# Performance work log

Measured on AMD Instinct MI355X. Metric: run time of the kernel, lower is better.

The kernel has to match this reference:

```python
import jax, jax.numpy as jnp
import numpy as np
from jax import lax

C = 512   # n_feat == Cn == Cdim (forced by DA_conv/CA_layer consistency)
H, W = 16, 32  # reshape_codebooks(512)
K = 3     # kernel_size
RED = 8   # reduction


def _lrelu(x):
    return jax.nn.leaky_relu(x, 0.1)


def _conv1x1(x, w, b=None):
    # x: (B,C,H,W), w: (O,C) -- torch Conv2d(.,.,1) weight squeezed
    y = jnp.einsum('oc,bchw->bohw', w, x)
    if b is not None:
        y = y + b[None, :, None, None]
    return y


def _conv3x3(x, w, b):
    # x: (B,C,H,W), w: (O,C,3,3) OIHW, padding=k//2 == SAME for odd k
    y = lax.conv_general_dilated(x, w, (1, 1), 'SAME',
                                 dimension_numbers=('NCHW', 'OIHW', 'NCHW'))
    return y + b[None, :, None, None]


def _da_conv(c, deg, kw1, kw2, pw, pb, caw1, caw2):
    # per-channel dynamic kernels from degradation vectors: (Cn, K*K)
    kern = (_lrelu(deg @ kw1.T) @ kw2.T).reshape(C, 1, K, K)
    # depthwise conv, groups = b1*c1 = C (b1 == 1)
    out = lax.conv_general_dilated(c, kern, (1, 1), 'SAME',
                                   feature_group_count=C,
                                   dimension_numbers=('NCHW', 'OIHW', 'NCHW'))
    out = _lrelu(out)
    out = _conv1x1(out, pw, pb)
    # CA_layer: deg reshaped to (1, Cn, 16, 32), channel attention, deg * att
    dr = deg.reshape(1, C, H, W)
    att = jax.nn.sigmoid(_conv1x1(_lrelu(_conv1x1(dr, caw1)), caw2))
    return out + dr * att


def setup_inputs() -> dict:
    key = jax.random.key(0)
    ks = jax.random.split(key, 16)
    n = lambda i, shape, s=0.05: jax.random.normal(ks[i], shape, dtype=jnp.float32) * s
    return dict(
        c=jax.random.normal(ks[0], (1, C, H, W), dtype=jnp.float32),
        deg=jax.random.normal(ks[1], (C, C), dtype=jnp.float32) * 0.1,
        k1_w1=n(2, (C, C)), k1_w2=n(3, (K * K, C)),
        p1_w=n(4, (C, C)), p1_b=jnp.zeros((C,), jnp.float32),
        ca1_w1=n(5, (C // RED, C)), ca1_w2=n(6, (C, C // RED)),
        conv1_w=n(7, (C, C, K, K)), conv1_b=jnp.zeros((C,), jnp.float32),
        k2_w1=n(8, (C, C)), k2_w2=n(9, (K * K, C)),
        p2_w=n(10, (C, C)), p2_b=jnp.zeros((C,), jnp.float32),
        ca2_w1=n(11, (C // RED, C)), ca2_w2=n(12, (C, C // RED)),
        conv2_w=n(13, (C, C, K, K)), conv2_b=jnp.zeros((C,), jnp.float32),
    )


def reference(c, deg, k1_w1, k1_w2, p1_w, p1_b, ca1_w1, ca1_w2,
              conv1_w, conv1_b, k2_w1, k2_w2, p2_w, p2_b,
              ca2_w1, ca2_w2, conv2_w, conv2_b):
    out = _lrelu(_da_conv(c, deg, k1_w1, k1_w2, p1_w, p1_b, ca1_w1, ca1_w2))
    out = _lrelu(_conv3x3(out, conv1_w, conv1_b))
    out = _lrelu(_da_conv(out, deg, k2_w1, k2_w2, p2_w, p2_b, ca2_w1, ca2_w2))
    return _conv3x3(out, conv2_w, conv2_b) + c
```

## Files before the change

kernel.cpp:

```cpp
#include <hip/hip_runtime.h>
#include <hip/hip_bf16.h>

typedef __attribute__((ext_vector_type(8))) unsigned short ushort8;
typedef __attribute__((ext_vector_type(8))) __bf16 bf16x8;
typedef __attribute__((ext_vector_type(4))) float f32x4;
typedef __attribute__((ext_vector_type(4))) unsigned short ushort4v;

__device__ __forceinline__ float lrelu_f(float v){ return v > 0.f ? v : 0.1f*v; }

__device__ __forceinline__ unsigned short f2bf(float v){
  unsigned u = __float_as_uint(v);
  unsigned r = (u + 0x7fffu + ((u>>16)&1u)) >> 16;
  return (unsigned short)r;
}
__device__ __forceinline__ float bf2f(unsigned short u){
  return __uint_as_float(((unsigned)u)<<16);
}

__device__ __forceinline__ void packq(const float* __restrict__ s,
                                      unsigned short* __restrict__ d, int i){
  const float4 v = ((const float4*)s)[i];
  ushort4v o; o.x=f2bf(v.x); o.y=f2bf(v.y); o.z=f2bf(v.z); o.w=f2bf(v.w);
  *(ushort4v*)(d + (size_t)i*4) = o;
}

__global__ __launch_bounds__(256) void k_pack_all(
  const float* __restrict__ k1_w1, const float* __restrict__ k2_w1,
  const float* __restrict__ p1_w,  const float* __restrict__ p2_w,
  const float* __restrict__ ca1_w1,const float* __restrict__ ca1_w2,
  const float* __restrict__ ca2_w1,const float* __restrict__ ca2_w2,
  const float* __restrict__ deg,   const float* __restrict__ conv1_w,
  const float* __restrict__ conv2_w,
  unsigned short* __restrict__ K1B, unsigned short* __restrict__ K2B,
  unsigned short* __restrict__ P1B, unsigned short* __restrict__ P2B,
  unsigned short* __restrict__ CA1A,unsigned short* __restrict__ CA1B,
  unsigned short* __restrict__ CA2A,unsigned short* __restrict__ CA2B,
  unsigned short* __restrict__ DEGB,unsigned short* __restrict__ DEGT,
  unsigned short* __restrict__ WB1, unsigned short* __restrict__ WB2){
  int i = blockIdx.x*256 + threadIdx.x;
  if (i < 65536){ packq(k1_w1, K1B, i); return; } i -= 65536;
  if (i < 65536){ packq(k2_w1, K2B, i); return; } i -= 65536;
  if (i < 65536){ packq(p1_w,  P1B, i); return; } i -= 65536;
  if (i < 65536){ packq(p2_w,  P2B, i); return; } i -= 65536;
  if (i < 8192){ packq(ca1_w1, CA1A, i); return; } i -= 8192;
  if (i < 8192){ packq(ca1_w2, CA1B, i); return; } i -= 8192;
  if (i < 8192){ packq(ca2_w1, CA2A, i); return; } i -= 8192;
  if (i < 8192){ packq(ca2_w2, CA2B, i); return; } i -= 8192;
  if (i < 65536){ packq(deg, DEGB, i); return; } i -= 65536;
  if (i < 65536){
    const int j = i*4; const int p = j>>9, c = j&511;
    ushort4v o;
    o.x = f2bf(deg[(size_t)(c+0)*512 + p]);
    o.y = f2bf(deg[(size_t)(c+1)*512 + p]);
    o.z = f2bf(deg[(size_t)(c+2)*512 + p]);
    o.w = f2bf(deg[(size_t)(c+3)*512 + p]);
    *(ushort4v*)(DEGT + (size_t)j) = o;
    return;
  } i -= 65536;
  if (i < 589824){
    const int o_ = i/1152; const int r4 = (i - o_*1152)*4;
    const int t = r4>>9; const int ci = r4&511;
    const float* s = conv1_w + (size_t)o_*4608;
    ushort4v o;
    o.x = f2bf(s[(ci+0)*9 + t]); o.y = f2bf(s[(ci+1)*9 + t]);
    o.z = f2bf(s[(ci+2)*9 + t]); o.w = f2bf(s[(ci+3)*9 + t]);
    *(ushort4v*)(WB1 + (size_t)o_*4608 + r4) = o;
    return;
  } i -= 589824;
  if (i < 589824){
    const int o_ = i/1152; const int r4 = (i - o_*1152)*4;
    const int t = r4>>9; const int ci = r4&511;
    const float* s = conv2_w + (size_t)o_*4608;
    ushort4v o;
    o.x = f2bf(s[(ci+0)*9 + t]); o.y = f2bf(s[(ci+1)*9 + t]);
    o.z = f2bf(s[(ci+2)*9 + t]); o.w = f2bf(s[(ci+3)*9 + t]);
    *(ushort4v*)(WB2 + (size_t)o_*4608 + r4) = o;
  }
}

__device__ __forceinline__ void gemm64(
    const unsigned short* __restrict__ A, const unsigned short* __restrict__ Bt,
    int m0, int n0, int K, int tid,
    unsigned short* lA, unsigned short* lB, f32x4 acc[2][2]){
  const int wid = tid>>6, lane = tid&63;
  const int srow = tid>>2, skb = tid&3;
  const unsigned short* gA = A  + (size_t)(m0+srow)*K + skb*8;
  const unsigned short* gB = Bt + (size_t)(n0+srow)*K + skb*8;
  const int soff = srow*32 + 8*(skb ^ (srow&3));
  const int wr = (wid>>1)*32, wc = (wid&1)*32;
  const int l15 = lane&15, lkb = lane>>4;
  int aoff[2], boff[2];
  #pragma unroll
  for (int s=0;s<2;s++){
    const int Ra = wr + s*16 + l15;
    aoff[s] = Ra*32 + 8*(lkb ^ (Ra&3));
    const int Rb = wc + s*16 + l15;
    boff[s] = Rb*32 + 8*(lkb ^ (Rb&3));
  }
  const int nst = K>>5;
  ushort8 ra = *(const ushort8*)gA;
  ushort8 rb = *(const ushort8*)gB;
  *(ushort8*)(lA + soff) = ra;
  *(ushort8*)(lB + soff) = rb;
  if (nst > 1){ ra = *(const ushort8*)(gA+32); rb = *(const ushort8*)(gB+32); }
  __syncthreads();
  for (int st=0; st<nst; ++st){
    const int cur = (st&1)*2048;
    bf16x8 af[2], bfr[2];
    #pragma unroll
    for (int s=0;s<2;s++){
      af[s]  = *(const bf16x8*)(lA + cur + aoff[s]);
      bfr[s] = *(const bf16x8*)(lB + cur + boff[s]);
    }
    if (st+1 < nst){
      const int nxt = ((st+1)&1)*2048;
      *(ushort8*)(lA + nxt + soff) = ra;
      *(ushort8*)(lB + nxt + soff) = rb;
      if (st+2 < nst){
        ra = *(const ushort8*)(gA + (size_t)(st+2)*32);
        rb = *(const ushort8*)(gB + (size_t)(st+2)*32);
      }
    }
    #pragma unroll
    for (int mi=0;mi<2;mi++)
      #pragma unroll
      for (int ni=0;ni<2;ni++)
        acc[mi][ni] = __builtin_amdgcn_mfma_f32_16x16x32_bf16(af[mi], bfr[ni], acc[mi][ni], 0,0,0);
    __syncthreads();
  }
}

__global__ __launch_bounds__(256) void k_prep(
    const unsigned short* __restrict__ DEGB, const unsigned short* __restrict__ DEGT,
    const unsigned short* __restrict__ K1B,  const unsigned short* __restrict__ K2B,
    const unsigned short* __restrict__ CA1A, const unsigned short* __restrict__ CA2A,
    const unsigned short* __restrict__ CA1B, const unsigned short* __restrict__ CA2B,
    const float* __restrict__ kw2a, const float* __restrict__ kw2b,
    float* __restrict__ KP1, float* __restrict__ KP2,
    float* __restrict__ ATT1, float* __restrict__ ATT2){
  __shared__ unsigned short lA[4096], lB[4096];
  __shared__ float kp[2][64][9];
  __shared__ unsigned short hid[4096];
  int bid = blockIdx.x;
  const int tid = threadIdx.x;
  const int wid = tid>>6, lane = tid&63;
  const int l15 = lane&15, lkb = lane>>4;

  if (bid < 128){
    const int b  = bid>>6;
    const int r6 = bid&63;
    const int it = r6>>3, jc = r6&7;
    const unsigned short* Bt = b ? K2B : K1B;
    const float* kw2 = b ? kw2b : kw2a;
    float* KP = b ? KP2 : KP1;
    f32x4 acc[2][2] = {};
    gemm64(DEGB, Bt, it*64, jc*64, 512, tid, lA, lB, acc);

    const int wr = (wid>>1)*32, wcl = wid&1;
    const int col0 = wcl*32 + l15, col1 = col0 + 16;
    float w0[9], w1[9];
    #pragma unroll
    for (int t=0;t<9;t++){
      w0[t] = kw2[t*512 + jc*64 + col0];
      w1[t] = kw2[t*512 + jc*64 + col1];
    }
    #pragma unroll
    for (int mi=0;mi<2;mi++)
      #pragma unroll
      for (int r=0;r<4;r++){
        const float v0 = lrelu_f(acc[mi][0][r]);
        const float v1 = lrelu_f(acc[mi][1][r]);
        const int row = wr + mi*16 + lkb*4 + r;
        #pragma unroll
        for (int t=0;t<9;t++){
          float p = v0*w0[t] + v1*w1[t];
          p += __shfl_xor(p,1); p += __shfl_xor(p,2);
          p += __shfl_xor(p,4); p += __shfl_xor(p,8);
          if (l15==0) kp[wcl][row][t] = p;
        }
      }
    __syncthreads();
    for (int i = tid; i < 576; i += 256){
      const int row = i/9, t = i - row*9;
      KP[((size_t)jc*512 + it*64 + row)*9 + t] = kp[0][row][t] + kp[1][row][t];
    }
  } else {
    bid -= 128;
    const int b  = bid>>6;
    const int r6 = bid&63;
    const int mt = r6>>3, pt = r6&7;
    const unsigned short* CAa = b ? CA2A : CA1A;
    const unsigned short* CAb = b ? CA2B : CA1B;
    float* ATT = b ? ATT2 : ATT1;
    f32x4 acc[2][2] = {};
    gemm64(DEGT, CAa, pt*64, 0, 512, tid, lA, lB, acc);

    const int wr = (wid>>1)*32, wc = (wid&1)*32;
    #pragma unroll
    for (int mi=0;mi<2;mi++)
      #pragma unroll
      for (int ni=0;ni<2;ni++)
        #pragma unroll
        for (int r=0;r<4;r++){
          const int row = wr + mi*16 + lkb*4 + r;
          const int col = wc + ni*16 + l15;
          hid[row*64 + 8*((col>>3) ^ (row&7)) + (col&7)] = f2bf(lrelu_f(acc[mi][ni][r]));
        }
    __syncthreads();
    const int arow = tid>>2, akb0 = (tid&3)*2;
    #pragma unroll
    for (int kk=0;kk<2;kk++){
      const int kb = akb0+kk;
      *(ushort8*)(lA + arow*64 + 8*(kb ^ (arow&7))) =
        *(const ushort8*)(CAb + (size_t)(mt*64+arow)*64 + kb*8);
    }
    __syncthreads();
    f32x4 a2[2][2] = {};
    #pragma unroll
    for (int h=0;h<2;h++){
      bf16x8 af2[2], bf2[2];
      #pragma unroll
      for (int mi=0;mi<2;mi++){
        const int Ra = wr + mi*16 + l15;
        af2[mi] = *(const bf16x8*)(lA + Ra*64 + 8*((h*4+lkb) ^ (Ra&7)));
      }
      #pragma unroll
      for (int ni=0;ni<2;ni++){
        const int Rb = wc + ni*16 + l15;
        bf2[ni] = *(const bf16x8*)(hid + Rb*64 + 8*((h*4+lkb) ^ (Rb&7)));
      }
      #pragma unroll
      for (int mi=0;mi<2;mi++)
        #pragma unroll
        for (int ni=0;ni<2;ni++)
          a2[mi][ni] = __builtin_amdgcn_mfma_f32_16x16x32_bf16(af2[mi], bf2[ni], a2[mi][ni], 0,0,0);
    }
    #pragma unroll
    for (int mi=0;mi<2;mi++)
      #pragma unroll
      for (int ni=0;ni<2;ni++)
        #pragma unroll
        for (int r=0;r<4;r++){
          const int row = mt*64 + wr + mi*16 + lkb*4 + r;
          const int col = pt*64 + wc + ni*16 + l15;
          ATT[(size_t)row*512 + col] = 1.f/(1.f + expf(-a2[mi][ni][r]));
        }
  }
}

__global__ __launch_bounds__(512) void k_dwconv(const float* __restrict__ x,
    const float* __restrict__ KP, unsigned short* __restrict__ yt){
  const int c = blockIdx.x;
  const int p = threadIdx.x;
  const int iy = p>>5, ix = p&31;
  __shared__ float plane[18*34];
  __shared__ float ks[9];
  for (int i=p;i<18*34;i+=512) plane[i]=0.f;
  if (p < 9){
    float s = 0.f;
    #pragma unroll
    for (int jc=0;jc<8;jc++) s += KP[((size_t)jc*512 + c)*9 + p];
    ks[p] = s;
  }
  __syncthreads();
  plane[(iy+1)*34 + ix+1] = x[c*512 + p];
  __syncthreads();
  float s = 0.f;
  #pragma unroll
  for (int dy=0;dy<3;dy++)
    #pragma unroll
    for (int dx=0;dx<3;dx++)
      s += plane[(iy+dy)*34 + ix+dx]*ks[dy*3+dx];
  yt[(size_t)p*512 + c] = f2bf(lrelu_f(s));
}

__global__ __launch_bounds__(512) void k_dwconv_red(const unsigned short* __restrict__ part,
    const float* __restrict__ bias, const float* __restrict__ KP,
    unsigned short* __restrict__ yt, int nchunks){
  const int c = blockIdx.x;
  const int p = threadIdx.x;
  const int iy = p>>5, ix = p&31;
  __shared__ float plane[18*34];
  __shared__ float ks[9];
  for (int i=p;i<18*34;i+=512) plane[i]=0.f;
  if (p < 9){
    float s = 0.f;
    #pragma unroll
    for (int jc=0;jc<8;jc++) s += KP[((size_t)jc*512 + c)*9 + p];
    ks[p] = s;
  }
  __syncthreads();
  if (p < 128){
    const float b = bias[c];
    float4 a4 = {b,b,b,b};
    for (int s=0;s<nchunks;s++){
      const ushort4v v = ((const ushort4v*)(part + (size_t)s*262144 + c*512))[p];
      a4.x += bf2f(v.x); a4.y += bf2f(v.y); a4.z += bf2f(v.z); a4.w += bf2f(v.w);
    }
    a4.x = lrelu_f(a4.x); a4.y = lrelu_f(a4.y);
    a4.z = lrelu_f(a4.z); a4.w = lrelu_f(a4.w);
    const int px0 = p*4;
    float* dst = &plane[((px0>>5)+1)*34 + (px0&31)+1];
    dst[0]=a4.x; dst[1]=a4.y; dst[2]=a4.z; dst[3]=a4.w;
  }
  __syncthreads();
  float s = 0.f;
  #pragma unroll
  for (int dy=0;dy<3;dy++)
    #pragma unroll
    for (int dx=0;dx<3;dx++)
      s += plane[(iy+dy)*34 + ix+dx]*ks[dy*3+dx];
  yt[(size_t)p*512 + c] = f2bf(lrelu_f(s));
}

__global__ __launch_bounds__(256) void k_pw(
    const unsigned short* __restrict__ A, const unsigned short* __restrict__ Bt,
    const float* __restrict__ bias,
    const float* __restrict__ E1, const float* __restrict__ E2,
    unsigned short* __restrict__ XT){
  __shared__ unsigned short lA[2][1024], lB[2][1024];
  __shared__ float tile[32][33];
  const int tid = threadIdx.x;
  const int wid = tid>>6, lane = tid&63;
  const int M0 = blockIdx.x*32, N0 = blockIdx.y*32;

  const int half = tid>>7;
  const int st_ = tid&127;
  const int srow = st_>>2, skb = st_&3;
  const unsigned short* gS = (half ? Bt + (size_t)(N0+srow)*512
                                   : A  + (size_t)(M0+srow)*512) + skb*8;
  unsigned short (*lS)[1024] = half ? lB : lA;
  const int soff = srow*32 + 8*(skb ^ (srow&3));

  const int wr = (wid>>1)*16, wc = (wid&1)*16;
  const int l15 = lane&15, lkb = lane>>4;
  const int Ra = wr + l15, Rb = wc + l15;
  const int aoff = Ra*32 + 8*(lkb ^ (Ra&3));
  const int boff = Rb*32 + 8*(lkb ^ (Rb&3));

  f32x4 acc = {};
  ushort8 r0 = *(const ushort8*)gS;
  *(ushort8*)(&lS[0][soff]) = r0;
  r0 = *(const ushort8*)(gS+32);
  __syncthreads();
  for (int st=0; st<16; ++st){
    const int cur = st&1;
    const bf16x8 af = *(const bf16x8*)(&lA[cur][aoff]);
    const bf16x8 bf = *(const bf16x8*)(&lB[cur][boff]);
    if (st+1 < 16){
      *(ushort8*)(&lS[cur^1][soff]) = r0;
      if (st+2 < 16) r0 = *(const ushort8*)(gS + (size_t)(st+2)*32);
    }
    acc = __builtin_amdgcn_mfma_f32_16x16x32_bf16(af, bf, acc, 0,0,0);
    __syncthreads();
  }

  #pragma unroll
  for (int r=0;r<4;r++){
    const int rl = wr + lkb*4 + r;
    const int cl = wc + l15;
    const int rr = M0 + rl, col = N0 + cl;
    float v = acc[r] + bias[rr] + E1[(size_t)rr*512+col]*E2[(size_t)rr*512+col];
    tile[rl][cl] = lrelu_f(v);
  }
  __syncthreads();
  const int pr = tid>>3, q = tid&7;
  ushort4v o;
  o.x = f2bf(tile[q*4+0][pr]); o.y = f2bf(tile[q*4+1][pr]);
  o.z = f2bf(tile[q*4+2][pr]); o.w = f2bf(tile[q*4+3][pr]);
  *(ushort4v*)(XT + (size_t)(N0+pr)*512 + M0 + q*4) = o;
}

template<int KCH>
__global__ __launch_bounds__(256) void k_mfma_conv(
    const unsigned short* __restrict__ WB,
    const unsigned short* __restrict__ XT,
    unsigned short* __restrict__ part){
  __shared__ unsigned short lA[2][4096];
  __shared__ unsigned short lB[2][8192];
  const int tid = threadIdx.x;
  const int wid = tid>>6, lane = tid&63;
  const int m0 = blockIdx.x*64, n0 = blockIdx.y*128;
  const int k0 = blockIdx.z*KCH;

  const int srow = tid>>2, skb = tid&3;
  const unsigned short* gA = WB + (size_t)(m0+srow)*4608 + k0 + skb*8;
  const int brow1 = srow + 64;
  const int p0 = n0 + srow, p1 = n0 + brow1;
  const int py0 = p0>>5, px0 = p0&31, py1 = p1>>5, px1 = p1&31;
  const int s7 = srow&7;
  const int soffA0 = srow*64 + 8*(skb ^ s7);
  const int soffA1 = srow*64 + 8*((skb+4) ^ s7);
  const int soffB00 = soffA0,            soffB01 = soffA1;
  const int soffB10 = brow1*64 + 8*(skb ^ s7);
  const int soffB11 = brow1*64 + 8*((skb+4) ^ s7);

  const int wr = (wid>>1)*32, wc = (wid&1)*64;
  const int l15 = lane&15, lkb = lane>>4;
  int aoff[2][2], boff[4][2];
  #pragma unroll
  for (int s=0;s<2;s++){
    const int Ra = wr + s*16 + l15;
    #pragma unroll
    for (int h=0;h<2;h++) aoff[s][h] = Ra*64 + 8*((lkb+4*h) ^ (Ra&7));
  }
  #pragma unroll
  for (int u=0;u<4;u++){
    const int Rb = wc + u*16 + l15;
    #pragma unroll
    for (int h=0;h<2;h++) boff[u][h] = Rb*64 + 8*((lkb+4*h) ^ (Rb&7));
  }

  auto ldB = [&](int st, int py, int px, ushort8& lo, ushort8& hi){
    const int k = k0 + st*64;
    const int t = k>>9;
    const int dy = t/3, dx = t - dy*3;
    const int yy = py + dy - 1, xx = px + dx - 1;
    lo = (ushort8){}; hi = (ushort8){};
    if ((unsigned)yy < 16u && (unsigned)xx < 32u){
      const unsigned short* b = XT + (size_t)(yy*32+xx)*512 + (k&511) + skb*8;
      lo = *(const ushort8*)b; hi = *(const ushort8*)(b+32);
    }
  };

  constexpr int NST = KCH/64;
  f32x4 acc[2][4] = {};
  ushort8 ra0 = *(const ushort8*)gA;
  ushort8 ra1 = *(const ushort8*)(gA+32);
  ushort8 b00,b01,b10,b11;
  ldB(0, py0, px0, b00, b01);
  ldB(0, py1, px1, b10, b11);
  *(ushort8*)(&lA[0][soffA0]) = ra0;  *(ushort8*)(&lA[0][soffA1]) = ra1;
  *(ushort8*)(&lB[0][soffB00]) = b00; *(ushort8*)(&lB[0][soffB01]) = b01;
  *(ushort8*)(&lB[0][soffB10]) = b10; *(ushort8*)(&lB[0][soffB11]) = b11;
  if (NST > 1){
    ra0 = *(const ushort8*)(gA+64); ra1 = *(const ushort8*)(gA+96);
    ldB(1, py0, px0, b00, b01);
    ldB(1, py1, px1, b10, b11);
  }
  __syncthreads();
  for (int st=0; st<NST; ++st){
    const int cur = st&1;
    bf16x8 af[2][2], bfr[4][2];
    #pragma unroll
    for (int s=0;s<2;s++)
      #pragma unroll
      for (int h=0;h<2;h++) af[s][h] = *(const bf16x8*)(&lA[cur][aoff[s][h]]);
    #pragma unroll
    for (int u=0;u<4;u++)
      #pragma unroll
      for (int h=0;h<2;h++) bfr[u][h] = *(const bf16x8*)(&lB[cur][boff[u][h]]);
    if (st+1 < NST){
      const int nxt = cur^1;
      *(ushort8*)(&lA[nxt][soffA0]) = ra0;  *(ushort8*)(&lA[nxt][soffA1]) = ra1;
      *(ushort8*)(&lB[nxt][soffB00]) = b00; *(ushort8*)(&lB[nxt][soffB01]) = b01;
      *(ushort8*)(&lB[nxt][soffB10]) = b10; *(ushort8*)(&lB[nxt][soffB11]) = b11;
      if (st+2 < NST){
        ra0 = *(const ushort8*)(gA + (size_t)(st+2)*64);
        ra1 = *(const ushort8*)(gA + (size_t)(st+2)*64 + 32);
        ldB(st+2, py0, px0, b00, b01);
        ldB(st+2, py1, px1, b10, b11);
      }
    }
    #pragma unroll
    for (int h=0;h<2;h++)
      #pragma unroll
      for (int s=0;s<2;s++)
        #pragma unroll
        for (int u=0;u<4;u++)
          acc[s][u] = __builtin_amdgcn_mfma_f32_16x16x32_bf16(af[s][h], bfr[u][h], acc[s][u], 0,0,0);
    __syncthreads();
  }

  unsigned short* pbase = part + (size_t)blockIdx.z*262144;
  #pragma unroll
  for (int s=0;s<2;s++)
    #pragma unroll
    for (int u=0;u<4;u++){
      const int row = m0 + wr + s*16 + lkb*4;
      const int col = n0 + wc + u*16 + l15;
      #pragma unroll
      for (int r=0;r<4;r++)
        pbase[(size_t)(row+r)*512 + col] = f2bf(acc[s][u][r]);
    }
}

__global__ __launch_bounds__(256) void k_reduce_final(const unsigned short* __restrict__ part,
    const float* __restrict__ bias, const float* __restrict__ res,
    float* __restrict__ y, int nchunks){
  const int i = blockIdx.x*256 + threadIdx.x;
  const int o = i>>7;
  const float b = bias[o];
  float4 a4 = {b,b,b,b};
  for (int s=0;s<nchunks;s++){
    const ushort4v v = ((const ushort4v*)part)[(size_t)s*65536 + i];
    a4.x += bf2f(v.x); a4.y += bf2f(v.y); a4.z += bf2f(v.z); a4.w += bf2f(v.w);
  }
  const float4 rv = ((const float4*)res)[i];
  a4.x += rv.x; a4.y += rv.y; a4.z += rv.z; a4.w += rv.w;
  ((float4*)y)[i] = a4;
}

extern "C" void kernel_launch(void* const* d_in, const int* in_sizes, int n_in,
                              void* d_out, int out_size, void* d_ws, size_t ws_size,
                              hipStream_t stream) {
  (void)in_sizes; (void)n_in; (void)out_size; (void)ws_size;
  const float* xin    = (const float*)d_in[0];
  const float* deg    = (const float*)d_in[1];
  const float* k1_w1  = (const float*)d_in[2];
  const float* k1_w2  = (const float*)d_in[3];
  const float* p1_w   = (const float*)d_in[4];
  const float* p1_b   = (const float*)d_in[5];
  const float* ca1_w1 = (const float*)d_in[6];
  const float* ca1_w2 = (const float*)d_in[7];
  const float* conv1_w= (const float*)d_in[8];
  const float* conv1_b= (const float*)d_in[9];
  const float* k2_w1  = (const float*)d_in[10];
  const float* k2_w2  = (const float*)d_in[11];
  const float* p2_w   = (const float*)d_in[12];
  const float* p2_b   = (const float*)d_in[13];
  const float* ca2_w1 = (const float*)d_in[14];
  const float* ca2_w2 = (const float*)d_in[15];
  const float* conv2_w= (const float*)d_in[16];
  const float* conv2_b= (const float*)d_in[17];
  float* out = (float*)d_out;

  const int NS = 18;

  float* ws = (float*)d_ws;
  unsigned short* PART = (unsigned short*)ws;
  ws += (size_t)NS*131072;
  float* KP1  = ws;  ws += 36864;
  float* KP2  = ws;  ws += 36864;
  float* ATT1 = ws;  ws += 262144;
  float* ATT2 = ws;  ws += 262144;
  unsigned short* DEGB = (unsigned short*)ws; ws += 131072;
  unsigned short* DEGT = (unsigned short*)ws; ws += 131072;
  unsigned short* K1B  = (unsigned short*)ws; ws += 131072;
  unsigned short* K2B  = (unsigned short*)ws; ws += 131072;
  unsigned short* P1B  = (unsigned short*)ws; ws += 131072;
  unsigned short* P2B  = (unsigned short*)ws; ws += 131072;
  unsigned short* CA1A = (unsigned short*)ws; ws += 16384;
  unsigned short* CA1B = (unsigned short*)ws; ws += 16384;
  unsigned short* CA2A = (unsigned short*)ws; ws += 16384;
  unsigned short* CA2B = (unsigned short*)ws; ws += 16384;
  unsigned short* DWLT = (unsigned short*)ws; ws += 131072;
  unsigned short* XT   = (unsigned short*)ws; ws += 131072;
  unsigned short* WB1  = (unsigned short*)ws; ws += 1179648;
  unsigned short* WB2  = (unsigned short*)ws; ws += 1179648;

  k_pack_all<<<6272,256,0,stream>>>(k1_w1,k2_w1,p1_w,p2_w,
      ca1_w1,ca1_w2,ca2_w1,ca2_w2, deg, conv1_w, conv2_w,
      K1B,K2B,P1B,P2B, CA1A,CA1B,CA2A,CA2B, DEGB,DEGT, WB1,WB2);

  k_prep<<<256,256,0,stream>>>(DEGB,DEGT, K1B,K2B, CA1A,CA2A, CA1B,CA2B,
      k1_w2,k2_w2, KP1,KP2, ATT1,ATT2);

  k_dwconv<<<512,512,0,stream>>>(xin, KP1, DWLT);
  k_pw<<<dim3(16,16),256,0,stream>>>(P1B, DWLT, p1_b, deg, ATT1, XT);
  k_mfma_conv<256><<<dim3(8,4,18),256,0,stream>>>(WB1, XT, PART);
  k_dwconv_red<<<512,512,0,stream>>>(PART, conv1_b, KP2, DWLT, NS);
  k_pw<<<dim3(16,16),256,0,stream>>>(P2B, DWLT, p2_b, deg, ATT2, XT);
  k_mfma_conv<256><<<dim3(8,4,18),256,0,stream>>>(WB2, XT, PART);
  k_reduce_final<<<256,256,0,stream>>>(PART, conv2_b, xin, out, NS);
}
```

Baseline: 87.80 us.

## Fuse all stages into one cooperative persistent kernel with grid syncs

```diff
diff --git a/kernel.cpp b/kernel.cpp
--- a/kernel.cpp
+++ b/kernel.cpp
@@ -1,5 +1,8 @@
 #include <hip/hip_runtime.h>
 #include <hip/hip_bf16.h>
+#include <hip/hip_cooperative_groups.h>
+
+namespace cg = cooperative_groups;
 
 typedef __attribute__((ext_vector_type(8))) unsigned short ushort8;
 typedef __attribute__((ext_vector_type(8))) __bf16 bf16x8;
@@ -24,59 +27,18 @@
   *(ushort4v*)(d + (size_t)i*4) = o;
 }
 
-__global__ __launch_bounds__(256) void k_pack_all(
-  const float* __restrict__ k1_w1, const float* __restrict__ k2_w1,
-  const float* __restrict__ p1_w,  const float* __restrict__ p2_w,
-  const float* __restrict__ ca1_w1,const float* __restrict__ ca1_w2,
-  const float* __restrict__ ca2_w1,const float* __restrict__ ca2_w2,
-  const float* __restrict__ deg,   const float* __restrict__ conv1_w,
-  const float* __restrict__ conv2_w,
-  unsigned short* __restrict__ K1B, unsigned short* __restrict__ K2B,
-  unsigned short* __restrict__ P1B, unsigned short* __restrict__ P2B,
-  unsigned short* __restrict__ CA1A,unsigned short* __restrict__ CA1B,
-  unsigned short* __restrict__ CA2A,unsigned short* __restrict__ CA2B,
-  unsigned short* __restrict__ DEGB,unsigned short* __restrict__ DEGT,
-  unsigned short* __restrict__ WB1, unsigned short* __restrict__ WB2){
-  int i = blockIdx.x*256 + threadIdx.x;
-  if (i < 65536){ packq(k1_w1, K1B, i); return; } i -= 65536;
-  if (i < 65536){ packq(k2_w1, K2B, i); return; } i -= 65536;
-  if (i < 65536){ packq(p1_w,  P1B, i); return; } i -= 65536;
-  if (i < 65536){ packq(p2_w,  P2B, i); return; } i -= 65536;
-  if (i < 8192){ packq(ca1_w1, CA1A, i); return; } i -= 8192;
-  if (i < 8192){ packq(ca1_w2, CA1B, i); return; } i -= 8192;
-  if (i < 8192){ packq(ca2_w1, CA2A, i); return; } i -= 8192;
-  if (i < 8192){ packq(ca2_w2, CA2B, i); return; } i -= 8192;
-  if (i < 65536){ packq(deg, DEGB, i); return; } i -= 65536;
-  if (i < 65536){
-    const int j = i*4; const int p = j>>9, c = j&511;
-    ushort4v o;
-    o.x = f2bf(deg[(size_t)(c+0)*512 + p]);
-    o.y = f2bf(deg[(size_t)(c+1)*512 + p]);
-    o.z = f2bf(deg[(size_t)(c+2)*512 + p]);
-    o.w = f2bf(deg[(size_t)(c+3)*512 + p]);
-    *(ushort4v*)(DEGT + (size_t)j) = o;
-    return;
-  } i -= 65536;
-  if (i < 589824){
-    const int o_ = i/1152; const int r4 = (i - o_*1152)*4;
-    const int t = r4>>9; const int ci = r4&511;
-    const float* s = conv1_w + (size_t)o_*4608;
-    ushort4v o;
-    o.x = f2bf(s[(ci+0)*9 + t]); o.y = f2bf(s[(ci+1)*9 + t]);
-    o.z = f2bf(s[(ci+2)*9 + t]); o.w = f2bf(s[(ci+3)*9 + t]);
-    *(ushort4v*)(WB1 + (size_t)o_*4608 + r4) = o;
-    return;
-  } i -= 589824;
-  if (i < 589824){
-    const int o_ = i/1152; const int r4 = (i - o_*1152)*4;
-    const int t = r4>>9; const int ci = r4&511;
-    const float* s = conv2_w + (size_t)o_*4608;
-    ushort4v o;
-    o.x = f2bf(s[(ci+0)*9 + t]); o.y = f2bf(s[(ci+1)*9 + t]);
-    o.z = f2bf(s[(ci+2)*9 + t]); o.w = f2bf(s[(ci+3)*9 + t]);
-    *(ushort4v*)(WB2 + (size_t)o_*4608 + r4) = o;
-  }
-}
+struct Prm {
+  const float *xin,*deg;
+  const float *k1_w1,*k1_w2,*p1_b,*conv1_b;
+  const float *k2_w1,*k2_w2,*p2_b,*conv2_b;
+  const float *p1_w,*p2_w,*ca1_w1,*ca1_w2,*ca2_w1,*ca2_w2,*conv1_w,*conv2_w;
+  float* out;
+  unsigned short *PART,*DEGB,*DEGT,*K1B,*K2B,*P1B,*P2B;
+  unsigned short *CA1A,*CA1B,*CA2A,*CA2B,*DWLT,*XT,*WB1,*WB2;
+  float *KP1,*KP2,*ATT1,*ATT2;
+};
+
+#define NT_TOTAL 65536
 
 __device__ __forceinline__ void gemm64(
     const unsigned short* __restrict__ A, const unsigned short* __restrict__ Bt,
@@ -130,17 +92,47 @@
   }
 }
 
-__global__ __launch_bounds__(256) void k_prep(
-    const unsigned short* __restrict__ DEGB, const unsigned short* __restrict__ DEGT,
-    const unsigned short* __restrict__ K1B,  const unsigned short* __restrict__ K2B,
-    const unsigned short* __restrict__ CA1A, const unsigned short* __restrict__ CA2A,
-    const unsigned short* __restrict__ CA1B, const unsigned short* __restrict__ CA2B,
-    const float* __restrict__ kw2a, const float* __restrict__ kw2b,
-    float* __restrict__ KP1, float* __restrict__ KP2,
-    float* __restrict__ ATT1, float* __restrict__ ATT2){
-  __shared__ unsigned short lA[4096], lB[4096];
-  __shared__ float kp[2][64][9];
-  __shared__ unsigned short hid[4096];
+__device__ __forceinline__ void ph_pack(const Prm& p){
+  const int g0 = blockIdx.x*256 + threadIdx.x;
+  for (int i = g0; i < 1605632; i += NT_TOTAL){
+    int j = i;
+    if (j < 65536){ packq(p.k1_w1, p.K1B, j); continue; } j -= 65536;
+    if (j < 65536){ packq(p.k2_w1, p.K2B, j); continue; } j -= 65536;
+    if (j < 65536){ packq(p.p1_w,  p.P1B, j); continue; } j -= 65536;
+    if (j < 65536){ packq(p.p2_w,  p.P2B, j); continue; } j -= 65536;
+    if (j < 8192){ packq(p.ca1_w1, p.CA1A, j); continue; } j -= 8192;
+    if (j < 8192){ packq(p.ca1_w2, p.CA1B, j); continue; } j -= 8192;
+    if (j < 8192){ packq(p.ca2_w1, p.CA2A, j); continue; } j -= 8192;
+    if (j < 8192){ packq(p.ca2_w2, p.CA2B, j); continue; } j -= 8192;
+    if (j < 65536){ packq(p.deg, p.DEGB, j); continue; } j -= 65536;
+    if (j < 65536){
+      const int q = j*4; const int px = q>>9, c = q&511;
+      ushort4v o;
+      o.x = f2bf(p.deg[(size_t)(c+0)*512 + px]);
+      o.y = f2bf(p.deg[(size_t)(c+1)*512 + px]);
+      o.z = f2bf(p.deg[(size_t)(c+2)*512 + px]);
+      o.w = f2bf(p.deg[(size_t)(c+3)*512 + px]);
+      *(ushort4v*)(p.DEGT + (size_t)q) = o;
+      continue;
+    } j -= 65536;
+    const float* src; unsigned short* dst;
+    if (j < 589824){ src = p.conv1_w; dst = p.WB1; }
+    else { j -= 589824; src = p.conv2_w; dst = p.WB2; }
+    const int o_ = j/1152; const int r4 = (j - o_*1152)*4;
+    const int t = r4>>9; const int ci = r4&511;
+    const float* s = src + (size_t)o_*4608;
+    ushort4v o;
+    o.x = f2bf(s[(ci+0)*9 + t]); o.y = f2bf(s[(ci+1)*9 + t]);
+    o.z = f2bf(s[(ci+2)*9 + t]); o.w = f2bf(s[(ci+3)*9 + t]);
+    *(ushort4v*)(dst + (size_t)o_*4608 + r4) = o;
+  }
+}
+
+__device__ __forceinline__ void ph_prep(const Prm& p, unsigned char* smem){
+  unsigned short* lA = (unsigned short*)smem;
+  unsigned short* lB = lA + 4096;
+  float* kpf = (float*)(smem + 16384);
+  unsigned short* hid = (unsigned short*)(smem + 21056);
   int bid = blockIdx.x;
   const int tid = threadIdx.x;
   const int wid = tid>>6, lane = tid&63;
@@ -150,11 +142,11 @@
     const int b  = bid>>6;
     const int r6 = bid&63;
     const int it = r6>>3, jc = r6&7;
-    const unsigned short* Bt = b ? K2B : K1B;
-    const float* kw2 = b ? kw2b : kw2a;
-    float* KP = b ? KP2 : KP1;
+    const unsigned short* Bt = b ? p.K2B : p.K1B;
+    const float* kw2 = b ? p.k2_w2 : p.k1_w2;
+    float* KP = b ? p.KP2 : p.KP1;
     f32x4 acc[2][2] = {};
-    gemm64(DEGB, Bt, it*64, jc*64, 512, tid, lA, lB, acc);
+    gemm64(p.DEGB, Bt, it*64, jc*64, 512, tid, lA, lB, acc);
 
     const int wr = (wid>>1)*32, wcl = wid&1;
     const int col0 = wcl*32 + l15, col1 = col0 + 16;
@@ -173,27 +165,27 @@
         const int row = wr + mi*16 + lkb*4 + r;
         #pragma unroll
         for (int t=0;t<9;t++){
-          float p = v0*w0[t] + v1*w1[t];
-          p += __shfl_xor(p,1); p += __shfl_xor(p,2);
-          p += __shfl_xor(p,4); p += __shfl_xor(p,8);
-          if (l15==0) kp[wcl][row][t] = p;
+          float q = v0*w0[t] + v1*w1[t];
+          q += __shfl_xor(q,1); q += __shfl_xor(q,2);
+          q += __shfl_xor(q,4); q += __shfl_xor(q,8);
+          if (l15==0) kpf[wcl*576 + row*9 + t] = q;
         }
       }
     __syncthreads();
     for (int i = tid; i < 576; i += 256){
       const int row = i/9, t = i - row*9;
-      KP[((size_t)jc*512 + it*64 + row)*9 + t] = kp[0][row][t] + kp[1][row][t];
+      KP[((size_t)jc*512 + it*64 + row)*9 + t] = kpf[row*9+t] + kpf[576 + row*9+t];
     }
   } else {
     bid -= 128;
     const int b  = bid>>6;
     const int r6 = bid&63;
     const int mt = r6>>3, pt = r6&7;
-    const unsigned short* CAa = b ? CA2A : CA1A;
-    const unsigned short* CAb = b ? CA2B : CA1B;
-    float* ATT = b ? ATT2 : ATT1;
+    const unsigned short* CAa = b ? p.CA2A : p.CA1A;
+    const unsigned short* CAb = b ? p.CA2B : p.CA1B;
+    float* ATT = b ? p.ATT2 : p.ATT1;
     f32x4 acc[2][2] = {};
-    gemm64(DEGT, CAa, pt*64, 0, 512, tid, lA, lB, acc);
+    gemm64(p.DEGT, CAa, pt*64, 0, 512, tid, lA, lB, acc);
 
     const int wr = (wid>>1)*32, wc = (wid&1)*32;
     #pragma unroll
@@ -248,88 +240,76 @@
   }
 }
 
-__global__ __launch_bounds__(512) void k_dwconv(const float* __restrict__ x,
-    const float* __restrict__ KP, unsigned short* __restrict__ yt){
-  const int c = blockIdx.x;
-  const int p = threadIdx.x;
-  const int iy = p>>5, ix = p&31;
-  __shared__ float plane[18*34];
-  __shared__ float ks[9];
-  for (int i=p;i<18*34;i+=512) plane[i]=0.f;
-  if (p < 9){
-    float s = 0.f;
-    #pragma unroll
-    for (int jc=0;jc<8;jc++) s += KP[((size_t)jc*512 + c)*9 + p];
-    ks[p] = s;
-  }
-  __syncthreads();
-  plane[(iy+1)*34 + ix+1] = x[c*512 + p];
-  __syncthreads();
-  float s = 0.f;
+template<int MODE>
+__device__ __forceinline__ void ph_dw(const Prm& p, const float* KP,
+    const float* bias, unsigned char* smem){
+  float* plane = (float*)smem;
+  float* ks = plane + 612;
+  const int tid = threadIdx.x;
+  for (int i=tid;i<612;i+=256) plane[i]=0.f;
   #pragma unroll
-  for (int dy=0;dy<3;dy++)
-    #pragma unroll
-    for (int dx=0;dx<3;dx++)
-      s += plane[(iy+dy)*34 + ix+dx]*ks[dy*3+dx];
-  yt[(size_t)p*512 + c] = f2bf(lrelu_f(s));
-}
-
-__global__ __launch_bounds__(512) void k_dwconv_red(const unsigned short* __restrict__ part,
-    const float* __restrict__ bias, const float* __restrict__ KP,
-    unsigned short* __restrict__ yt, int nchunks){
-  const int c = blockIdx.x;
-  const int p = threadIdx.x;
-  const int iy = p>>5, ix = p&31;
-  __shared__ float plane[18*34];
-  __shared__ float ks[9];
-  for (int i=p;i<18*34;i+=512) plane[i]=0.f;
-  if (p < 9){
-    float s = 0.f;
-    #pragma unroll
-    for (int jc=0;jc<8;jc++) s += KP[((size_t)jc*512 + c)*9 + p];
-    ks[p] = s;
-  }
-  __syncthreads();
-  if (p < 128){
-    const float b = bias[c];
-    float4 a4 = {b,b,b,b};
-    for (int s=0;s<nchunks;s++){
-      const ushort4v v = ((const ushort4v*)(part + (size_t)s*262144 + c*512))[p];
-      a4.x += bf2f(v.x); a4.y += bf2f(v.y); a4.z += bf2f(v.z); a4.w += bf2f(v.w);
-    }
-    a4.x = lrelu_f(a4.x); a4.y = lrelu_f(a4.y);
-    a4.z = lrelu_f(a4.z); a4.w = lrelu_f(a4.w);
-    const int px0 = p*4;
-    float* dst = &plane[((px0>>5)+1)*34 + (px0&31)+1];
-    dst[0]=a4.x; dst[1]=a4.y; dst[2]=a4.z; dst[3]=a4.w;
-  }
-  __syncthreads();
-  float s = 0.f;
-  #pragma unroll
-  for (int dy=0;dy<3;dy++)
-    #pragma unroll
-    for (int dx=0;dx<3;dx++)
-      s += plane[(iy+dy)*34 + ix+dx]*ks[dy*3+dx];
-  yt[(size_t)p*512 + c] = f2bf(lrelu_f(s));
-}
-
-__global__ __launch_bounds__(256) void k_pw(
-    const unsigned short* __restrict__ A, const unsigned short* __restrict__ Bt,
-    const float* __restrict__ bias,
-    const float* __restrict__ E1, const float* __restrict__ E2,
-    unsigned short* __restrict__ XT){
-  __shared__ unsigned short lA[2][1024], lB[2][1024];
-  __shared__ float tile[32][33];
+  for (int cc=0; cc<2; ++cc){
+    const int c = blockIdx.x*2 + cc;
+    __syncthreads();
+    if (tid<9){
+      float s=0.f;
+      #pragma unroll
+      for (int jc=0;jc<8;jc++) s += KP[((size_t)jc*512 + c)*9 + tid];
+      ks[tid]=s;
+    }
+    if constexpr (MODE==0){
+      #pragma unroll
+      for (int q=0;q<2;q++){
+        const int px = tid + q*256;
+        plane[((px>>5)+1)*34 + (px&31)+1] = p.xin[(size_t)c*512 + px];
+      }
+    } else {
+      if (tid < 128){
+        const float b = bias[c];
+        float4 a4 = {b,b,b,b};
+        #pragma unroll
+        for (int s=0;s<4;s++){
+          const ushort4v v = ((const ushort4v*)(p.PART + (size_t)s*262144 + c*512))[tid];
+          a4.x += bf2f(v.x); a4.y += bf2f(v.y); a4.z += bf2f(v.z); a4.w += bf2f(v.w);
+        }
+        a4.x = lrelu_f(a4.x); a4.y = lrelu_f(a4.y);
+        a4.z = lrelu_f(a4.z); a4.w = lrelu_f(a4.w);
+        const int px0 = tid*4;
+        float* dst = &plane[((px0>>5)+1)*34 + (px0&31)+1];
+        dst[0]=a4.x; dst[1]=a4.y; dst[2]=a4.z; dst[3]=a4.w;
+      }
+    }
+    __syncthreads();
+    #pragma unroll
+    for (int q=0;q<2;q++){
+      const int px = tid + q*256;
+      const int iy = px>>5, ix = px&31;
+      float s = 0.f;
+      #pragma unroll
+      for (int dy=0;dy<3;dy++)
+        #pragma unroll
+        for (int dx=0;dx<3;dx++)
+          s += plane[(iy+dy)*34 + ix+dx]*ks[dy*3+dx];
+      p.DWLT[(size_t)px*512 + c] = f2bf(lrelu_f(s));
+    }
+  }
+}
+
+__device__ __forceinline__ void ph_pw(const Prm& p, const unsigned short* A,
+    const float* bias, const float* ATT, unsigned char* smem){
+  unsigned short* lA = (unsigned short*)smem;
+  unsigned short* lB = lA + 2048;
+  float* tile = (float*)(smem + 8192);
   const int tid = threadIdx.x;
   const int wid = tid>>6, lane = tid&63;
-  const int M0 = blockIdx.x*32, N0 = blockIdx.y*32;
+  const int M0 = (blockIdx.x&15)*32, N0 = (blockIdx.x>>4)*32;
 
   const int half = tid>>7;
   const int st_ = tid&127;
   const int srow = st_>>2, skb = st_&3;
-  const unsigned short* gS = (half ? Bt + (size_t)(N0+srow)*512
-                                   : A  + (size_t)(M0+srow)*512) + skb*8;
-  unsigned short (*lS)[1024] = half ? lB : lA;
+  const unsigned short* gS = (half ? p.DWLT + (size_t)(N0+srow)*512
+                                   : A      + (size_t)(M0+srow)*512) + skb*8;
+  unsigned short* lS = half ? lB : lA;
   const int soff = srow*32 + 8*(skb ^ (srow&3));
 
   const int wr = (wid>>1)*16, wc = (wid&1)*16;
@@ -340,15 +320,15 @@
 
   f32x4 acc = {};
   ushort8 r0 = *(const ushort8*)gS;
-  *(ushort8*)(&lS[0][soff]) = r0;
+  *(ushort8*)(lS + soff) = r0;
   r0 = *(const ushort8*)(gS+32);
   __syncthreads();
   for (int st=0; st<16; ++st){
-    const int cur = st&1;
-    const bf16x8 af = *(const bf16x8*)(&lA[cur][aoff]);
-    const bf16x8 bf = *(const bf16x8*)(&lB[cur][boff]);
+    const int cur = (st&1)*1024;
+    const bf16x8 af = *(const bf16x8*)(lA + cur + aoff);
+    const bf16x8 bf = *(const bf16x8*)(lB + cur + boff);
     if (st+1 < 16){
-      *(ushort8*)(&lS[cur^1][soff]) = r0;
+      *(ushort8*)(lS + (cur^1024) + soff) = r0;
       if (st+2 < 16) r0 = *(const ushort8*)(gS + (size_t)(st+2)*32);
     }
     acc = __builtin_amdgcn_mfma_f32_16x16x32_bf16(af, bf, acc, 0,0,0);
@@ -360,207 +340,221 @@
     const int rl = wr + lkb*4 + r;
     const int cl = wc + l15;
     const int rr = M0 + rl, col = N0 + cl;
-    float v = acc[r] + bias[rr] + E1[(size_t)rr*512+col]*E2[(size_t)rr*512+col];
-    tile[rl][cl] = lrelu_f(v);
+    float v = acc[r] + bias[rr] + p.deg[(size_t)rr*512+col]*ATT[(size_t)rr*512+col];
+    tile[rl*33 + cl] = lrelu_f(v);
   }
   __syncthreads();
   const int pr = tid>>3, q = tid&7;
   ushort4v o;
-  o.x = f2bf(tile[q*4+0][pr]); o.y = f2bf(tile[q*4+1][pr]);
-  o.z = f2bf(tile[q*4+2][pr]); o.w = f2bf(tile[q*4+3][pr]);
-  *(ushort4v*)(XT + (size_t)(N0+pr)*512 + M0 + q*4) = o;
-}
-
-template<int KCH>
-__global__ __launch_bounds__(256) void k_mfma_conv(
-    const unsigned short* __restrict__ WB,
-    const unsigned short* __restrict__ XT,
-    unsigned short* __restrict__ part){
-  __shared__ unsigned short lA[2][4096];
-  __shared__ unsigned short lB[2][8192];
+  o.x = f2bf(tile[(q*4+0)*33 + pr]); o.y = f2bf(tile[(q*4+1)*33 + pr]);
+  o.z = f2bf(tile[(q*4+2)*33 + pr]); o.w = f2bf(tile[(q*4+3)*33 + pr]);
+  *(ushort4v*)(p.XT + (size_t)(N0+pr)*512 + M0 + q*4) = o;
+}
+
+__device__ __forceinline__ void ph_conv(const Prm& p, const unsigned short* WB,
+    unsigned char* smem){
+  unsigned short* lA = (unsigned short*)smem;
+  unsigned short* lB = lA + 8192;
   const int tid = threadIdx.x;
+  const int bid = blockIdx.x;
+  const int z = bid & 3, ny = (bid>>2)&7, mx = bid>>5;
+  const int m0 = mx*64, n0 = ny*64, k0 = z*1152;
   const int wid = tid>>6, lane = tid&63;
-  const int m0 = blockIdx.x*64, n0 = blockIdx.y*128;
-  const int k0 = blockIdx.z*KCH;
-
   const int srow = tid>>2, skb = tid&3;
   const unsigned short* gA = WB + (size_t)(m0+srow)*4608 + k0 + skb*8;
-  const int brow1 = srow + 64;
-  const int p0 = n0 + srow, p1 = n0 + brow1;
-  const int py0 = p0>>5, px0 = p0&31, py1 = p1>>5, px1 = p1&31;
+  const int pp = n0 + srow, py = pp>>5, px = pp&31;
   const int s7 = srow&7;
-  const int soffA0 = srow*64 + 8*(skb ^ s7);
-  const int soffA1 = srow*64 + 8*((skb+4) ^ s7);
-  const int soffB00 = soffA0,            soffB01 = soffA1;
-  const int soffB10 = brow1*64 + 8*(skb ^ s7);
-  const int soffB11 = brow1*64 + 8*((skb+4) ^ s7);
-
-  const int wr = (wid>>1)*32, wc = (wid&1)*64;
+  const int soff0 = srow*64 + 8*(skb ^ s7);
+  const int soff1 = srow*64 + 8*((skb+4) ^ s7);
+
+  const int wr = (wid>>1)*32, wc = (wid&1)*32;
   const int l15 = lane&15, lkb = lane>>4;
-  int aoff[2][2], boff[4][2];
+  int aoff[2][2], boff[2][2];
   #pragma unroll
   for (int s=0;s<2;s++){
     const int Ra = wr + s*16 + l15;
-    #pragma unroll
-    for (int h=0;h<2;h++) aoff[s][h] = Ra*64 + 8*((lkb+4*h) ^ (Ra&7));
-  }
-  #pragma unroll
-  for (int u=0;u<4;u++){
-    const int Rb = wc + u*16 + l15;
-    #pragma unroll
-    for (int h=0;h<2;h++) boff[u][h] = Rb*64 + 8*((lkb+4*h) ^ (Rb&7));
-  }
-
-  auto ldB = [&](int st, int py, int px, ushort8& lo, ushort8& hi){
+    const int Rb = wc + s*16 + l15;
+    #pragma unroll
+    for (int h=0;h<2;h++){
+      aoff[s][h] = Ra*64 + 8*((lkb+4*h) ^ (Ra&7));
+      boff[s][h] = Rb*64 + 8*((lkb+4*h) ^ (Rb&7));
+    }
+  }
+
+  auto ldB = [&](int st, ushort8& lo, ushort8& hi){
     const int k = k0 + st*64;
     const int t = k>>9;
     const int dy = t/3, dx = t - dy*3;
     const int yy = py + dy - 1, xx = px + dx - 1;
     lo = (ushort8){}; hi = (ushort8){};
     if ((unsigned)yy < 16u && (unsigned)xx < 32u){
-      const unsigned short* b = XT + (size_t)(yy*32+xx)*512 + (k&511) + skb*8;
+      const unsigned short* b = p.XT + (size_t)(yy*32+xx)*512 + (k&511) + skb*8;
       lo = *(const ushort8*)b; hi = *(const ushort8*)(b+32);
     }
   };
 
-  constexpr int NST = KCH/64;
-  f32x4 acc[2][4] = {};
+  constexpr int NST = 18;
+  f32x4 acc[2][2] = {};
   ushort8 ra0 = *(const ushort8*)gA;
   ushort8 ra1 = *(const ushort8*)(gA+32);
-  ushort8 b00,b01,b10,b11;
-  ldB(0, py0, px0, b00, b01);
-  ldB(0, py1, px1, b10, b11);
-  *(ushort8*)(&lA[0][soffA0]) = ra0;  *(ushort8*)(&lA[0][soffA1]) = ra1;
-  *(ushort8*)(&lB[0][soffB00]) = b00; *(ushort8*)(&lB[0][soffB01]) = b01;
-  *(ushort8*)(&lB[0][soffB10]) = b10; *(ushort8*)(&lB[0][soffB11]) = b11;
-  if (NST > 1){
-    ra0 = *(const ushort8*)(gA+64); ra1 = *(const ushort8*)(gA+96);
-    ldB(1, py0, px0, b00, b01);
-    ldB(1, py1, px1, b10, b11);
-  }
+  ushort8 b0, b1;
+  ldB(0, b0, b1);
+  *(ushort8*)(lA + soff0) = ra0; *(ushort8*)(lA + soff1) = ra1;
+  *(ushort8*)(lB + soff0) = b0;  *(ushort8*)(lB + soff1) = b1;
+  ra0 = *(const ushort8*)(gA+64); ra1 = *(const ushort8*)(gA+96);
+  ldB(1, b0, b1);
   __syncthreads();
   for (int st=0; st<NST; ++st){
-    const int cur = st&1;
-    bf16x8 af[2][2], bfr[4][2];
+    const int cur = (st&1)*4096;
+    bf16x8 af[2][2], bfr[2][2];
     #pragma unroll
     for (int s=0;s<2;s++)
       #pragma unroll
-      for (int h=0;h<2;h++) af[s][h] = *(const bf16x8*)(&lA[cur][aoff[s][h]]);
-    #pragma unroll
-    for (int u=0;u<4;u++)
-      #pragma unroll
-      for (int h=0;h<2;h++) bfr[u][h] = *(const bf16x8*)(&lB[cur][boff[u][h]]);
+      for (int h=0;h<2;h++){
+        af[s][h]  = *(const bf16x8*)(lA + cur + aoff[s][h]);
+        bfr[s][h] = *(const bf16x8*)(lB + cur + boff[s][h]);
+      }
     if (st+1 < NST){
-      const int nxt = cur^1;
-      *(ushort8*)(&lA[nxt][soffA0]) = ra0;  *(ushort8*)(&lA[nxt][soffA1]) = ra1;
-      *(ushort8*)(&lB[nxt][soffB00]) = b00; *(ushort8*)(&lB[nxt][soffB01]) = b01;
-      *(ushort8*)(&lB[nxt][soffB10]) = b10; *(ushort8*)(&lB[nxt][soffB11]) = b11;
+      const int nxt = cur ^ 4096;
+      *(ushort8*)(lA + nxt + soff0) = ra0; *(ushort8*)(lA + nxt + soff1) = ra1;
+      *(ushort8*)(lB + nxt + soff0) = b0;  *(ushort8*)(lB + nxt + soff1) = b1;
       if (st+2 < NST){
         ra0 = *(const ushort8*)(gA + (size_t)(st+2)*64);
         ra1 = *(const ushort8*)(gA + (size_t)(st+2)*64 + 32);
-        ldB(st+2, py0, px0, b00, b01);
-        ldB(st+2, py1, px1, b10, b11);
+        ldB(st+2, b0, b1);
       }
     }
     #pragma unroll
     for (int h=0;h<2;h++)
       #pragma unroll
-      for (int s=0;s<2;s++)
-        #pragma unroll
-        for (int u=0;u<4;u++)
-          acc[s][u] = __builtin_amdgcn_mfma_f32_16x16x32_bf16(af[s][h], bfr[u][h], acc[s][u], 0,0,0);
-    __syncthreads();
-  }
-
-  unsigned short* pbase = part + (size_t)blockIdx.z*262144;
+      for (int mi=0;mi<2;mi++)
+        #pragma unroll
+        for (int ni=0;ni<2;ni++)
+          acc[mi][ni] = __builtin_amdgcn_mfma_f32_16x16x32_bf16(af[mi][h], bfr[ni][h], acc[mi][ni], 0,0,0);
+    __syncthreads();
+  }
+
+  unsigned short* pbase = p.PART + (size_t)z*262144;
   #pragma unroll
-  for (int s=0;s<2;s++)
-    #pragma unroll
-    for (int u=0;u<4;u++){
-      const int row = m0 + wr + s*16 + lkb*4;
-      const int col = n0 + wc + u*16 + l15;
+  for (int mi=0;mi<2;mi++)
+    #pragma unroll
+    for (int ni=0;ni<2;ni++){
+      const int row = m0 + wr + mi*16 + lkb*4;
+      const int col = n0 + wc + ni*16 + l15;
       #pragma unroll
       for (int r=0;r<4;r++)
-        pbase[(size_t)(row+r)*512 + col] = f2bf(acc[s][u][r]);
-    }
-}
-
-__global__ __launch_bounds__(256) void k_reduce_final(const unsigned short* __restrict__ part,
-    const float* __restrict__ bias, const float* __restrict__ res,
-    float* __restrict__ y, int nchunks){
-  const int i = blockIdx.x*256 + threadIdx.x;
-  const int o = i>>7;
-  const float b = bias[o];
+        pbase[(size_t)(row+r)*512 + col] = f2bf(acc[mi][ni][r]);
+    }
+}
+
+__device__ __forceinline__ void ph_reduce(const Prm& p){
+  const int gid = blockIdx.x*256 + threadIdx.x;
+  const int o = gid>>7;
+  const float b = p.conv2_b[o];
   float4 a4 = {b,b,b,b};
-  for (int s=0;s<nchunks;s++){
-    const ushort4v v = ((const ushort4v*)part)[(size_t)s*65536 + i];
+  #pragma unroll
+  for (int s=0;s<4;s++){
+    const ushort4v v = ((const ushort4v*)p.PART)[(size_t)s*65536 + gid];
     a4.x += bf2f(v.x); a4.y += bf2f(v.y); a4.z += bf2f(v.z); a4.w += bf2f(v.w);
   }
-  const float4 rv = ((const float4*)res)[i];
+  const float4 rv = ((const float4*)p.xin)[gid];
   a4.x += rv.x; a4.y += rv.y; a4.z += rv.z; a4.w += rv.w;
-  ((float4*)y)[i] = a4;
-}
+  ((float4*)p.out)[gid] = a4;
+}
+
+__global__ __launch_bounds__(256) void k_mega(Prm p){
+  cg::grid_group grid = cg::this_grid();
+  __shared__ __align__(16) unsigned char smem[32768];
+
+  ph_pack(p);                                   grid.sync();
+  ph_prep(p, smem);                             grid.sync();
+  ph_dw<0>(p, p.KP1, nullptr, smem);            grid.sync();
+  ph_pw(p, p.P1B, p.p1_b, p.ATT1, smem);        grid.sync();
+  ph_conv(p, p.WB1, smem);                      grid.sync();
+  ph_dw<1>(p, p.KP2, p.conv1_b, smem);          grid.sync();
+  ph_pw(p, p.P2B, p.p2_b, p.ATT2, smem);        grid.sync();
+  ph_conv(p, p.WB2, smem);                      grid.sync();
+  ph_reduce(p);
+}
+
+__global__ __launch_bounds__(256) void kw_pack(Prm p){ ph_pack(p); }
+__global__ __launch_bounds__(256) void kw_prep(Prm p){
+  __shared__ __align__(16) unsigned char s[32768]; ph_prep(p, s); }
+template<int M>
+__global__ __launch_bounds__(256) void kw_dw(Prm p){
+  __shared__ __align__(16) unsigned char s[4096];
+  if constexpr (M==0) ph_dw<0>(p, p.KP1, nullptr, s);
+  else                ph_dw<1>(p, p.KP2, p.conv1_b, s); }
+template<int W>
+__global__ __launch_bounds__(256) void kw_pw(Prm p){
+  __shared__ __align__(16) unsigned char s[16384];
+  if constexpr (W==0) ph_pw(p, p.P1B, p.p1_b, p.ATT1, s);
+  else                ph_pw(p, p.P2B, p.p2_b, p.ATT2, s); }
+template<int W>
+__global__ __launch_bounds__(256) void kw_conv(Prm p){
+  __shared__ __align__(16) unsigned char s[32768];
+  ph_conv(p, W ? p.WB2 : p.WB1, s); }
+__global__ __launch_bounds__(256) void kw_reduce(Prm p){ ph_reduce(p); }
 
 extern "C" void kernel_launch(void* const* d_in, const int* in_sizes, int n_in,
                               void* d_out, int out_size, void* d_ws, size_t ws_size,
                               hipStream_t stream) {
   (void)in_sizes; (void)n_in; (void)out_size; (void)ws_size;
-  const float* xin    = (const float*)d_in[0];
-  const float* deg    = (const float*)d_in[1];
-  const float* k1_w1  = (const float*)d_in[2];
-  const float* k1_w2  = (const float*)d_in[3];
-  const float* p1_w   = (const float*)d_in[4];
-  const float* p1_b   = (const float*)d_in[5];
-  const float* ca1_w1 = (const float*)d_in[6];
-  const float* ca1_w2 = (const float*)d_in[7];
-  const float* conv1_w= (const float*)d_in[8];
-  const float* conv1_b= (const float*)d_in[9];
-  const float* k2_w1  = (const float*)d_in[10];
-  const float* k2_w2  = (const float*)d_in[11];
-  const float* p2_w   = (const float*)d_in[12];
-  const float* p2_b   = (const float*)d_in[13];
-  const float* ca2_w1 = (const float*)d_in[14];
-  const float* ca2_w2 = (const float*)d_in[15];
-  const float* conv2_w= (const float*)d_in[16];
-  const float* conv2_b= (const float*)d_in[17];
-  float* out = (float*)d_out;
-
-  const int NS = 18;
+  Prm p;
+  p.xin    = (const float*)d_in[0];
+  p.deg    = (const float*)d_in[1];
+  p.k1_w1  = (const float*)d_in[2];
+  p.k1_w2  = (const float*)d_in[3];
+  p.p1_w   = (const float*)d_in[4];
+  p.p1_b   = (const float*)d_in[5];
+  p.ca1_w1 = (const float*)d_in[6];
+  p.ca1_w2 = (const float*)d_in[7];
+  p.conv1_w= (const float*)d_in[8];
+  p.conv1_b= (const float*)d_in[9];
+  p.k2_w1  = (const float*)d_in[10];
+  p.k2_w2  = (const float*)d_in[11];
+  p.p2_w   = (const float*)d_in[12];
+  p.p2_b   = (const float*)d_in[13];
+  p.ca2_w1 = (const float*)d_in[14];
+  p.ca2_w2 = (const float*)d_in[15];
+  p.conv2_w= (const float*)d_in[16];
+  p.conv2_b= (const float*)d_in[17];
+  p.out    = (float*)d_out;
 
   float* ws = (float*)d_ws;
-  unsigned short* PART = (unsigned short*)ws;
-  ws += (size_t)NS*131072;
-  float* KP1  = ws;  ws += 36864;
-  float* KP2  = ws;  ws += 36864;
-  float* ATT1 = ws;  ws += 262144;
-  float* ATT2 = ws;  ws += 262144;
-  unsigned short* DEGB = (unsigned short*)ws; ws += 131072;
-  unsigned short* DEGT = (unsigned short*)ws; ws += 131072;
-  unsigned short* K1B  = (unsigned short*)ws; ws += 131072;
-  unsigned short* K2B  = (unsigned short*)ws; ws += 131072;
-  unsigned short* P1B  = (unsigned short*)ws; ws += 131072;
-  unsigned short* P2B  = (unsigned short*)ws; ws += 131072;
-  unsigned short* CA1A = (unsigned short*)ws; ws += 16384;
-  unsigned short* CA1B = (unsigned short*)ws; ws += 16384;
-  unsigned short* CA2A = (unsigned short*)ws; ws += 16384;
-  unsigned short* CA2B = (unsigned short*)ws; ws += 16384;
-  unsigned short* DWLT = (unsigned short*)ws; ws += 131072;
-  unsigned short* XT   = (unsigned short*)ws; ws += 131072;
-  unsigned short* WB1  = (unsigned short*)ws; ws += 1179648;
-  unsigned short* WB2  = (unsigned short*)ws; ws += 1179648;
-
-  k_pack_all<<<6272,256,0,stream>>>(k1_w1,k2_w1,p1_w,p2_w,
-      ca1_w1,ca1_w2,ca2_w1,ca2_w2, deg, conv1_w, conv2_w,
-      K1B,K2B,P1B,P2B, CA1A,CA1B,CA2A,CA2B, DEGB,DEGT, WB1,WB2);
-
-  k_prep<<<256,256,0,stream>>>(DEGB,DEGT, K1B,K2B, CA1A,CA2A, CA1B,CA2B,
-      k1_w2,k2_w2, KP1,KP2, ATT1,ATT2);
-
-  k_dwconv<<<512,512,0,stream>>>(xin, KP1, DWLT);
-  k_pw<<<dim3(16,16),256,0,stream>>>(P1B, DWLT, p1_b, deg, ATT1, XT);
-  k_mfma_conv<256><<<dim3(8,4,18),256,0,stream>>>(WB1, XT, PART);
-  k_dwconv_red<<<512,512,0,stream>>>(PART, conv1_b, KP2, DWLT, NS);
-  k_pw<<<dim3(16,16),256,0,stream>>>(P2B, DWLT, p2_b, deg, ATT2, XT);
-  k_mfma_conv<256><<<dim3(8,4,18),256,0,stream>>>(WB2, XT, PART);
-  k_reduce_final<<<256,256,0,stream>>>(PART, conv2_b, xin, out, NS);
-}
+  p.PART = (unsigned short*)ws;  ws += 524288;
+  p.KP1  = ws;  ws += 36864;
+  p.KP2  = ws;  ws += 36864;
+  p.ATT1 = ws;  ws += 262144;
+  p.ATT2 = ws;  ws += 262144;
+  p.DEGB = (unsigned short*)ws; ws += 131072;
+  p.DEGT = (unsigned short*)ws; ws += 131072;
+  p.K1B  = (unsigned short*)ws; ws += 131072;
+  p.K2B  = (unsigned short*)ws; ws += 131072;
+  p.P1B  = (unsigned short*)ws; ws += 131072;
+  p.P2B  = (unsigned short*)ws; ws += 131072;
+  p.CA1A = (unsigned short*)ws; ws += 16384;
+  p.CA1B = (unsigned short*)ws; ws += 16384;
+  p.CA2A = (unsigned short*)ws; ws += 16384;
+  p.CA2B = (unsigned short*)ws; ws += 16384;
+  p.DWLT = (unsigned short*)ws; ws += 131072;
+  p.XT   = (unsigned short*)ws; ws += 131072;
+  p.WB1  = (unsigned short*)ws; ws += 1179648;
+  p.WB2  = (unsigned short*)ws; ws += 1179648;
+
+  void* kargs[] = { &p };
+  hipError_t e = hipLaunchCooperativeKernel((void*)k_mega, dim3(256), dim3(256),
+                                            kargs, 0, stream);
+  if (e != hipSuccess){
+    (void)hipGetLastError();
+    kw_pack   <<<256,256,0,stream>>>(p);
+    kw_prep   <<<256,256,0,stream>>>(p);
+    kw_dw<0>  <<<256,256,0,stream>>>(p);
+    kw_pw<0>  <<<256,256,0,stream>>>(p);
+    kw_conv<0><<<256,256,0,stream>>>(p);
+    kw_dw<1>  <<<256,256,0,stream>>>(p);
+    kw_pw<1>  <<<256,256,0,stream>>>(p);
+    kw_conv<1><<<256,256,0,stream>>>(p);
+    kw_reduce <<<256,256,0,stream>>>(p);
+  }
+}
```

After: 326.8 us. 272% more time.
